# Optimization experiments

Hardware: AMD Instinct MI355X
Metric: run time of the kernel (lower is better)

## Reference

```python
import jax, jax.numpy as jnp
import numpy as np

N = 50000
E_RAND = 800000
IN_CH = 128
HID = 64
HEADS = 4
OUT_CH = 3
NEG_SLOPE = 0.2
BN_EPS = 1e-5


def setup_inputs() -> dict:
    key = jax.random.key(0)
    ks = jax.random.split(key, 24)
    x = jax.random.normal(ks[0], (N, IN_CH), dtype=jnp.float32)
    er = jax.random.randint(ks[1], (2, E_RAND), 0, N)
    sl = jnp.tile(jnp.arange(N, dtype=er.dtype)[None, :], (2, 1))
    edge_index = jnp.concatenate([er, sl], axis=1)  # [2, 850000]
    s = 0.1
    d1 = HID * HEADS            # 256
    d2 = (HID // 2) * HEADS     # 128
    inp = dict(x=x, edge_index=edge_index)
    # layer 1: in 128 -> heads*64
    inp["W1"] = s * jax.random.normal(ks[2], (IN_CH, HEADS * HID), dtype=jnp.float32)
    inp["a1s"] = s * jax.random.normal(ks[3], (HEADS, HID), dtype=jnp.float32)
    inp["a1d"] = s * jax.random.normal(ks[4], (HEADS, HID), dtype=jnp.float32)
    inp["b1"] = jnp.zeros((d1,), jnp.float32)
    inp["g1"] = jnp.ones((d1,), jnp.float32)
    inp["be1"] = jnp.zeros((d1,), jnp.float32)
    inp["m1"] = 0.01 * jax.random.normal(ks[5], (d1,), dtype=jnp.float32)
    inp["v1"] = jnp.ones((d1,), jnp.float32) + 0.01 * jax.random.uniform(ks[6], (d1,))
    # layer 2: in 256 -> heads*32
    inp["W2"] = s * jax.random.normal(ks[7], (d1, HEADS * (HID // 2)), dtype=jnp.float32)
    inp["a2s"] = s * jax.random.normal(ks[8], (HEADS, HID // 2), dtype=jnp.float32)
    inp["a2d"] = s * jax.random.normal(ks[9], (HEADS, HID // 2), dtype=jnp.float32)
    inp["b2"] = jnp.zeros((d2,), jnp.float32)
    inp["g2"] = jnp.ones((d2,), jnp.float32)
    inp["be2"] = jnp.zeros((d2,), jnp.float32)
    inp["m2"] = 0.01 * jax.random.normal(ks[10], (d2,), dtype=jnp.float32)
    inp["v2"] = jnp.ones((d2,), jnp.float32) + 0.01 * jax.random.uniform(ks[11], (d2,))
    # layer 3: in 128 -> 1 head, out_ch, concat=False
    inp["W3"] = s * jax.random.normal(ks[12], (d2, OUT_CH), dtype=jnp.float32)
    inp["a3s"] = s * jax.random.normal(ks[13], (1, OUT_CH), dtype=jnp.float32)
    inp["a3d"] = s * jax.random.normal(ks[14], (1, OUT_CH), dtype=jnp.float32)
    inp["b3"] = jnp.zeros((OUT_CH,), jnp.float32)
    return inp


def gat_conv(x, src, dst, W, a_src, a_dst, b, heads, fdim, concat):
    n = x.shape[0]
    h = (x @ W).reshape(n, heads, fdim)           # [N,H,F]
    als = jnp.einsum('nhf,hf->nh', h, a_src)      # [N,H]
    ald = jnp.einsum('nhf,hf->nh', h, a_dst)
    e = jax.nn.leaky_relu(als[src] + ald[dst], NEG_SLOPE)  # [E,H]
    m = jax.lax.stop_gradient(jax.ops.segment_max(e, dst, num_segments=n))
    ex = jnp.exp(e - m[dst])
    ssum = jax.ops.segment_sum(ex, dst, num_segments=n)
    alpha = ex / (ssum[dst] + 1e-16)              # segment softmax over in-edges
    msg = h[src] * alpha[:, :, None]              # [E,H,F]
    out = jax.ops.segment_sum(msg, dst, num_segments=n)  # [N,H,F]
    out = out.reshape(n, heads * fdim) if concat else out.mean(axis=1)
    return out + b


def batch_norm(x, gamma, beta, mean, var):
    return (x - mean) * jax.lax.rsqrt(var + BN_EPS) * gamma + beta


def reference(x, edge_index, W1, a1s, a1d, b1, g1, be1, m1, v1,
              W2, a2s, a2d, b2, g2, be2, m2, v2,
              W3, a3s, a3d, b3):
    src, dst = edge_index[0], edge_index[1]
    h = gat_conv(x, src, dst, W1, a1s, a1d, b1, HEADS, HID, True)
    h = jax.nn.elu(batch_norm(h, g1, be1, m1, v1))
    h = gat_conv(h, src, dst, W2, a2s, a2d, b2, HEADS, HID // 2, True)
    h = jax.nn.elu(batch_norm(h, g2, be2, m2, v2))
    h = gat_conv(h, src, dst, W3, a3s, a3d, b3, 1, OUT_CH, False)
    return jax.nn.log_softmax(h, axis=1)
```

## Files before the change

### kernel.cpp

```cpp
#include <hip/hip_runtime.h>


#define WSZ 64

typedef short short8 __attribute__((ext_vector_type(8)));
typedef short short4v __attribute__((ext_vector_type(4)));
typedef float float4v __attribute__((ext_vector_type(4)));
typedef float f2v __attribute__((ext_vector_type(2)));
typedef unsigned uint2v __attribute__((ext_vector_type(2)));

__device__ inline unsigned short f2bf(float f) {
  unsigned u = __float_as_uint(f);
  u += 0x7FFFu + ((u >> 16) & 1u);
  return (unsigned short)(u >> 16);
}
__device__ inline float bf2f(unsigned short u) {
  return __uint_as_float(((unsigned)u) << 16);
}


__global__ __launch_bounds__(256) void hist_kernel(const int* __restrict__ dst, int E,
                                                   int* __restrict__ deg) {
  int e = blockIdx.x * 256 + threadIdx.x;
  if (e < E) atomicAdd(&deg[dst[e]], 1);
}

__global__ __launch_bounds__(256) void block_sums_kernel(const int* __restrict__ deg, int n,
                                                         int* __restrict__ bsum) {
  __shared__ int sh[256];
  int t = threadIdx.x;
  int base = blockIdx.x * 1024 + t * 4;
  int v = 0;
#pragma unroll
  for (int j = 0; j < 4; ++j) {
    int idx = base + j;
    if (idx < n) v += deg[idx];
  }
  sh[t] = v;
  __syncthreads();
  for (int off = 128; off >= 1; off >>= 1) {
    if (t < off) sh[t] += sh[t + off];
    __syncthreads();
  }
  if (t == 0) bsum[blockIdx.x] = sh[0];
}

__global__ void tiny_scan_kernel(int* bsum, int nb) {
  if (threadIdx.x == 0 && blockIdx.x == 0) {
    int run = 0;
    for (int i = 0; i < nb; ++i) {
      int v = bsum[i];
      bsum[i] = run;
      run += v;
    }
  }
}

__global__ __launch_bounds__(256) void scan_write_kernel(const int* __restrict__ deg, int n,
                                                         const int* __restrict__ bbase,
                                                         int* __restrict__ row_start,
                                                         int* __restrict__ cursor) {
  __shared__ int sh[256];
  int t = threadIdx.x;
  int base = blockIdx.x * 1024 + t * 4;
  int v[4];
  int s = 0;
#pragma unroll
  for (int j = 0; j < 4; ++j) {
    int idx = base + j;
    v[j] = (idx < n) ? deg[idx] : 0;
    s += v[j];
  }
  sh[t] = s;
  __syncthreads();
  for (int off = 1; off < 256; off <<= 1) {
    int x = (t >= off) ? sh[t - off] : 0;
    __syncthreads();
    sh[t] += x;
    __syncthreads();
  }
  int excl = sh[t] - s + bbase[blockIdx.x];
#pragma unroll
  for (int j = 0; j < 4; ++j) {
    int idx = base + j;
    if (idx < n) {
      row_start[idx] = excl;
      cursor[idx] = excl;
    }
    excl += v[j];
  }
  if (blockIdx.x == gridDim.x - 1 && t == 255) row_start[n] = excl;
}

__global__ __launch_bounds__(256) void scatter_kernel(const int* __restrict__ src,
                                                      const int* __restrict__ dst, int E,
                                                      int* __restrict__ cursor,
                                                      int* __restrict__ csr_src) {
  int e = blockIdx.x * 256 + threadIdx.x;
  if (e < E) {
    int d = dst[e];
    int p = atomicAdd(&cursor[d], 1);
    csr_src[p] = src[e];
  }
}


__global__ __launch_bounds__(256) void conv_w1t_kernel(const float* __restrict__ W1,
                                                       unsigned short* __restrict__ W1t) {
  int idx = blockIdx.x * 256 + threadIdx.x;
  int n = idx >> 7, k = idx & 127;
  W1t[idx] = f2bf(W1[k * 256 + n]);
}

__global__ __launch_bounds__(256) void conv_w2t_kernel(const float* __restrict__ W2,
                                                       unsigned short* __restrict__ W2t) {
  int idx = blockIdx.x * 256 + threadIdx.x;
  int n = idx >> 8, p = idx & 255;
  int kl = (p & ~63) | ((p & 3) << 4) | ((p >> 2) & 15);
  W2t[idx] = f2bf(W2[kl * 128 + n]);
}

__global__ __launch_bounds__(512) void bn_prep_kernel(
    const float* __restrict__ b1, const float* __restrict__ g1,
    const float* __restrict__ be1, const float* __restrict__ m1,
    const float* __restrict__ v1, const float* __restrict__ b2,
    const float* __restrict__ g2, const float* __restrict__ be2,
    const float* __restrict__ m2, const float* __restrict__ v2,
    float* __restrict__ sc1, float* __restrict__ sh1,
    float* __restrict__ sc2, float* __restrict__ sh2) {
  int t = threadIdx.x;
  if (t < 256) {
    float s = g1[t] * rsqrtf(v1[t] + 1e-5f);
    sc1[t] = s;
    sh1[t] = (b1[t] - m1[t]) * s + be1[t];
  } else if (t < 384) {
    int i = t - 256;
    float s = g2[i] * rsqrtf(v2[i] + 1e-5f);
    sc2[i] = s;
    sh2[i] = (b2[i] - m2[i]) * s + be2[i];
  }
}


template <int K, int BN, bool AF32>
__global__ __launch_bounds__(256) void gemm_mfma(
    const void* __restrict__ Ap,
    const unsigned short* __restrict__ Bt,
    const float* __restrict__ a_s, const float* __restrict__ a_d,
    unsigned short* __restrict__ hout,
    float* __restrict__ als, float* __restrict__ ald,
    int M) {
  constexpr int CF = BN / 64;
  constexpr int SF = BN / 8;
  constexpr int PAD = 36;
  __shared__ unsigned short As[64][PAD];
  __shared__ unsigned short Bs[BN][PAD];
  const int t = threadIdx.x;
  const int w = t >> 6;
  const int lane = t & 63;
  const int c16 = lane & 15;
  const int q = lane >> 4;
  const int bm = blockIdx.x * 64;
  const int arow = t >> 2;
  const int akc = (t & 3) * 8;

  float4v acc[4][CF];
#pragma unroll
  for (int rf = 0; rf < 4; ++rf)
#pragma unroll
    for (int cf = 0; cf < CF; ++cf) acc[rf][cf] = float4v{0.f, 0.f, 0.f, 0.f};

  for (int k0 = 0; k0 < K; k0 += 32) {
    {
      int gr = bm + arow;
      if constexpr (AF32) {
        const float* Af = (const float*)Ap + (size_t)gr * K + k0 + akc;
        float4 v0 = make_float4(0.f, 0.f, 0.f, 0.f), v1 = v0;
        if (gr < M) {
          v0 = *(const float4*)Af;
          v1 = *(const float4*)(Af + 4);
        }
        ushort4 u0, u1;
        u0.x = f2bf(v0.x); u0.y = f2bf(v0.y); u0.z = f2bf(v0.z); u0.w = f2bf(v0.w);
        u1.x = f2bf(v1.x); u1.y = f2bf(v1.y); u1.z = f2bf(v1.z); u1.w = f2bf(v1.w);
        *(ushort4*)&As[arow][akc] = u0;
        *(ushort4*)&As[arow][akc + 4] = u1;
      } else {
        uint4 v = make_uint4(0u, 0u, 0u, 0u);
        if (gr < M) v = *(const uint4*)((const unsigned short*)Ap + (size_t)gr * K + k0 + akc);
        *(uint2*)&As[arow][akc] = make_uint2(v.x, v.y);
        *(uint2*)&As[arow][akc + 4] = make_uint2(v.z, v.w);
      }
    }
#pragma unroll
    for (int h = 0; h < BN / 64; ++h) {
      int n = (t >> 2) + h * 64;
      uint4 v = *(const uint4*)(Bt + (size_t)n * K + k0 + akc);
      *(uint2*)&Bs[n][akc] = make_uint2(v.x, v.y);
      *(uint2*)&Bs[n][akc + 4] = make_uint2(v.z, v.w);
    }
    __syncthreads();
    short8 af[4], bfr[CF];
#pragma unroll
    for (int rf = 0; rf < 4; ++rf) {
      short4v lo = *(short4v*)&As[rf * 16 + c16][q * 8];
      short4v hi = *(short4v*)&As[rf * 16 + c16][q * 8 + 4];
      af[rf] = __builtin_shufflevector(lo, hi, 0, 1, 2, 3, 4, 5, 6, 7);
    }
#pragma unroll
    for (int cf = 0; cf < CF; ++cf) {
      int n = w * (CF * 16) + cf * 16 + c16;
      short4v lo = *(short4v*)&Bs[n][q * 8];
      short4v hi = *(short4v*)&Bs[n][q * 8 + 4];
      bfr[cf] = __builtin_shufflevector(lo, hi, 0, 1, 2, 3, 4, 5, 6, 7);
    }
#pragma unroll
    for (int rf = 0; rf < 4; ++rf)
#pragma unroll
      for (int cf = 0; cf < CF; ++cf)
        acc[rf][cf] =
            __builtin_amdgcn_mfma_f32_16x16x32_bf16(af[rf], bfr[cf], acc[rf][cf], 0, 0, 0);
    __syncthreads();
  }

  float sasv[CF], sadv[CF];
#pragma unroll
  for (int cf = 0; cf < CF; ++cf) {
    int L = w * (CF * 16) + cf * 16 + c16;
    sasv[cf] = a_s[L];
    sadv[cf] = a_d[L];
  }
  const size_t sub = (size_t)(w * 2 + (c16 >> 3)) * (size_t)M * SF;
#pragma unroll
  for (int rf = 0; rf < 4; ++rf) {
#pragma unroll
    for (int r = 0; r < 4; ++r) {
      int n = bm + rf * 16 + q * 4 + r;
      float ps = 0.f, pd = 0.f;
      unsigned short us[CF];
#pragma unroll
      for (int cf = 0; cf < CF; ++cf) {
        float v = acc[rf][cf][r];
        us[cf] = f2bf(v);
        ps += v * sasv[cf];
        pd += v * sadv[cf];
      }
#pragma unroll
      for (int off = 1; off <= 8; off <<= 1) {
        ps += __shfl_xor(ps, off, 16);
        pd += __shfl_xor(pd, off, 16);
      }
      if (n < M) {
        if constexpr (CF == 4) {
          ushort4 u;
          u.x = us[0]; u.y = us[1]; u.z = us[2]; u.w = us[3];
          *(ushort4*)(hout + sub + (size_t)n * 32 + (c16 & 7) * 4) = u;
        } else {
          ushort2 u;
          u.x = us[0]; u.y = us[1];
          *(ushort2*)(hout + sub + (size_t)n * 16 + (c16 & 7) * 2) = u;
        }
        if (c16 == 0) {
          als[(size_t)n * 4 + w] = ps;
          ald[(size_t)n * 4 + w] = pd;
        }
      }
    }
  }
}


__global__ __launch_bounds__(256) void alpha_kernel(
    const float* __restrict__ als, const float* __restrict__ ald,
    const int* __restrict__ row_start, const int* __restrict__ csr_src,
    float* __restrict__ alpha, int E, int n_nodes) {
  int wid = threadIdx.x >> 6, lane = threadIdx.x & 63;
  int n = __builtin_amdgcn_readfirstlane(blockIdx.x * 4 + wid);
  if (n >= n_nodes) return;
  int head = lane & 3;
  int eg = lane >> 2;
  float aldv = ald[(size_t)n * 4 + head];
  int row = __builtin_amdgcn_readfirstlane(row_start[n]);
  int end = __builtin_amdgcn_readfirstlane(row_start[n + 1]);
  float ssum = 0.f;
  for (int i = row; i < end; i += 16) {
    int e = i + eg;
    int ec = (e < end) ? e : (end - 1);
    int s = csr_src[ec];
    float x = als[(size_t)(unsigned)s * 4 + head] + aldv;
    x = fmaxf(x, 0.2f * x);
    float ex = __expf(x);
    ssum += (e < end) ? ex : 0.f;
  }
  ssum += __shfl_xor(ssum, 4, 64);
  ssum += __shfl_xor(ssum, 8, 64);
  ssum += __shfl_xor(ssum, 16, 64);
  ssum += __shfl_xor(ssum, 32, 64);
  float inv = 1.f / (ssum + 1e-16f);
  float* apl = alpha + (size_t)head * (unsigned)E;
  for (int i = row; i < end; i += 16) {
    int e = i + eg;
    if (e < end) {
      int s = csr_src[e];
      float x = als[(size_t)(unsigned)s * 4 + head] + aldv;
      x = fmaxf(x, 0.2f * x);
      apl[e] = __expf(x) * inv;
    }
  }
}


template <int D>
__global__ __launch_bounds__(256) void gat_agg_slice(
    const unsigned short* __restrict__ h_sl,
    const float* __restrict__ alpha,
    const int* __restrict__ row_start, const int* __restrict__ csr_src,
    const float* __restrict__ bnsc, const float* __restrict__ bnsh,
    unsigned short* __restrict__ obf,
    float* __restrict__ of32,
    int E, int n_nodes) {
  constexpr int SFEAT = D / 8;
  constexpr int KF = SFEAT / 8;
  const int sl = blockIdx.x & 7;
  const int g = blockIdx.x >> 3;
  const int wid = threadIdx.x >> 6, lane = threadIdx.x & 63;
  const int f = lane & 7;
  const int ng = lane >> 3;
  const int head = sl >> 1;
  const char* hb = (const char*)(h_sl + (size_t)sl * (unsigned)n_nodes * SFEAT);
  const char* cb = (const char*)csr_src;
  const char* apb = (const char*)(alpha + (size_t)head * (unsigned)E);
  const unsigned uoff = (unsigned)(f * KF * 2);

  const int lb = (D == 256 ? head * 64 : head * 32) + (sl & 1) * 8 + f;
  float sc0 = bnsc[lb], sh0 = bnsh[lb];
  float sc1 = bnsc[lb + 16], sh1 = bnsh[lb + 16];
  float sc2 = 0.f, sh2 = 0.f, sc3 = 0.f, sh3 = 0.f;
  if constexpr (D == 256) {
    sc2 = bnsc[lb + 32]; sh2 = bnsh[lb + 32];
    sc3 = bnsc[lb + 48]; sh3 = bnsh[lb + 48];
  }

  int n = g * 32 + wid * 8 + ng;
  bool valid = n < n_nodes;
  int nc = valid ? n : (n_nodes - 1);
  int row = row_start[nc];
  int deg = row_start[nc + 1] - row;
  if (!valid) deg = 0;
  int mx = deg;
#pragma unroll
  for (int off = 8; off <= 32; off <<= 1) mx = max(mx, __shfl_xor(mx, off, 64));
  mx = __builtin_amdgcn_readfirstlane(mx);

  float acc0 = 0.f, acc1 = 0.f, acc2 = 0.f, acc3 = 0.f;
#pragma unroll 2
  for (int j = 0; j < mx; ++j) {
    bool act = j < deg;
    unsigned idx = (unsigned)(row + (act ? j : 0));
    int s = *(const int*)(cb + idx * 4u);
    float a = *(const float*)(apb + idx * 4u);
    a = act ? a : 0.f;
    if constexpr (D == 256) {
      uint2v u = *(const uint2v*)(hb + ((unsigned)s * 64u + uoff));
      acc0 += a * __uint_as_float(u.x << 16);
      acc1 += a * __uint_as_float(u.x & 0xffff0000u);
      acc2 += a * __uint_as_float(u.y << 16);
      acc3 += a * __uint_as_float(u.y & 0xffff0000u);
    } else {
      unsigned u = *(const unsigned*)(hb + ((unsigned)s * 32u + uoff));
      acc0 += a * __uint_as_float(u << 16);
      acc1 += a * __uint_as_float(u & 0xffff0000u);
    }
  }

  if (valid) {
    if constexpr (D == 256) {
      float v0 = acc0 * sc0 + sh0;
      float v1 = acc1 * sc1 + sh1;
      float v2 = acc2 * sc2 + sh2;
      float v3 = acc3 * sc3 + sh3;
      v0 = (v0 > 0.f) ? v0 : (__expf(v0) - 1.f);
      v1 = (v1 > 0.f) ? v1 : (__expf(v1) - 1.f);
      v2 = (v2 > 0.f) ? v2 : (__expf(v2) - 1.f);
      v3 = (v3 > 0.f) ? v3 : (__expf(v3) - 1.f);
      uint2v pk;
      pk.x = (unsigned)f2bf(v0) | ((unsigned)f2bf(v1) << 16);
      pk.y = (unsigned)f2bf(v2) | ((unsigned)f2bf(v3) << 16);
      __builtin_nontemporal_store(
          pk, (uint2v*)(obf + (size_t)n * 256 + sl * 32 + f * 4));
    } else {
      float v0 = acc0 * sc0 + sh0;
      float v1 = acc1 * sc1 + sh1;
      v0 = (v0 > 0.f) ? v0 : (__expf(v0) - 1.f);
      v1 = (v1 > 0.f) ? v1 : (__expf(v1) - 1.f);
      f2v v2;
      v2.x = v0; v2.y = v1;
      __builtin_nontemporal_store(
          v2, (f2v*)(of32 + (size_t)n * 128 + sl * 16 + f * 2));
    }
  }
}


__global__ __launch_bounds__(256) void l3_prep_kernel(
    const float* __restrict__ o2, const float* __restrict__ W3,
    const float* __restrict__ a3s, const float* __restrict__ a3d,
    float4* __restrict__ h3p, float* __restrict__ ald3, int n_nodes) {
  __shared__ float w3s[384];
  __shared__ float sa3[6];
  for (int i = threadIdx.x; i < 384; i += 256) w3s[i] = W3[i];
  if (threadIdx.x < 3) {
    sa3[threadIdx.x] = a3s[threadIdx.x];
    sa3[3 + threadIdx.x] = a3d[threadIdx.x];
  }
  __syncthreads();
  int wid = threadIdx.x >> 6, lane = threadIdx.x & 63;
  int n = blockIdx.x * 4 + wid;
  if (n >= n_nodes) return;
  f2v v = *(const f2v*)(o2 + (size_t)n * 128 + lane * 2);
  int hd = lane >> 4;
  int k0l = hd * 32 + (lane & 15);
  int k1l = k0l + 16;
  float p0 = v.x * w3s[k0l * 3 + 0] + v.y * w3s[k1l * 3 + 0];
  float p1 = v.x * w3s[k0l * 3 + 1] + v.y * w3s[k1l * 3 + 1];
  float p2 = v.x * w3s[k0l * 3 + 2] + v.y * w3s[k1l * 3 + 2];
#pragma unroll
  for (int off = 32; off >= 1; off >>= 1) {
    p0 += __shfl_xor(p0, off, 64);
    p1 += __shfl_xor(p1, off, 64);
    p2 += __shfl_xor(p2, off, 64);
  }
  if (lane == 0) {
    float als3 = p0 * sa3[0] + p1 * sa3[1] + p2 * sa3[2];
    float ad3 = p0 * sa3[3] + p1 * sa3[4] + p2 * sa3[5];
    h3p[n] = make_float4(p0, p1, p2, als3);
    ald3[n] = ad3;
  }
}


__global__ __launch_bounds__(256) void l3_agg_kernel(const float4* __restrict__ h3p,
                                                     const float* __restrict__ ald3,
                                                     const int* __restrict__ row_start,
                                                     const int* __restrict__ csr_src,
                                                     const float* __restrict__ b3,
                                                     float* __restrict__ out, int n_nodes) {
  int wid = threadIdx.x >> 6, lane = threadIdx.x & 63;
  int n = __builtin_amdgcn_readfirstlane(blockIdx.x * 4 + wid);
  if (n >= n_nodes) return;
  float aldv = ald3[n];
  int row = __builtin_amdgcn_readfirstlane(row_start[n]);
  int end = __builtin_amdgcn_readfirstlane(row_start[n + 1]);
  const char* hp = (const char*)h3p;
  float a0 = 0.f, a1 = 0.f, a2 = 0.f, ss = 0.f;
  for (int i = row + lane; i < end; i += 64) {
    int s = csr_src[i];
    float4 hv = *(const float4*)(hp + ((unsigned)s * 16u));
    float e = hv.w + aldv;
    e = fmaxf(e, 0.2f * e);
    float ex = __expf(e);
    ss += ex;
    a0 += ex * hv.x;
    a1 += ex * hv.y;
    a2 += ex * hv.z;
  }
#pragma unroll
  for (int off = 32; off >= 1; off >>= 1) {
    a0 += __shfl_xor(a0, off, 64);
    a1 += __shfl_xor(a1, off, 64);
    a2 += __shfl_xor(a2, off, 64);
    ss += __shfl_xor(ss, off, 64);
  }
  if (lane == 0) {
    float inv = 1.f / (ss + 1e-16f);
    float o0 = a0 * inv + b3[0];
    float o1 = a1 * inv + b3[1];
    float o2 = a2 * inv + b3[2];
    float m = fmaxf(o0, fmaxf(o1, o2));
    float lse = m + logf(expf(o0 - m) + expf(o1 - m) + expf(o2 - m));
    out[n * 3 + 0] = o0 - lse;
    out[n * 3 + 1] = o1 - lse;
    out[n * 3 + 2] = o2 - lse;
  }
}


extern "C" void kernel_launch(void* const* d_in, const int* in_sizes, int n_in,
                              void* d_out, int out_size, void* d_ws, size_t ws_size,
                              hipStream_t stream) {
  const float* x   = (const float*)d_in[0];
  const int*   ei  = (const int*)d_in[1];
  const float* W1  = (const float*)d_in[2];
  const float* a1s = (const float*)d_in[3];
  const float* a1d = (const float*)d_in[4];
  const float* b1  = (const float*)d_in[5];
  const float* g1v = (const float*)d_in[6];
  const float* be1 = (const float*)d_in[7];
  const float* m1  = (const float*)d_in[8];
  const float* v1  = (const float*)d_in[9];
  const float* W2  = (const float*)d_in[10];
  const float* a2s = (const float*)d_in[11];
  const float* a2d = (const float*)d_in[12];
  const float* b2  = (const float*)d_in[13];
  const float* g2v = (const float*)d_in[14];
  const float* be2 = (const float*)d_in[15];
  const float* m2  = (const float*)d_in[16];
  const float* v2  = (const float*)d_in[17];
  const float* W3  = (const float*)d_in[18];
  const float* a3s = (const float*)d_in[19];
  const float* a3d = (const float*)d_in[20];
  const float* b3  = (const float*)d_in[21];
  float* out = (float*)d_out;

  const int N = in_sizes[0] / 128;
  const int E = in_sizes[1] / 2;
  const int* srcv = ei;
  const int* dstv = ei + E;

  float* wsf  = (float*)d_ws;
  float* als1 = wsf;
  float* ald1 = als1 + (size_t)N * 4;
  float* als2 = ald1 + (size_t)N * 4;
  float* ald2 = als2 + (size_t)N * 4;
  float* h3p  = ald2 + (size_t)N * 4;
  float* ald3 = h3p + (size_t)N * 4;
  unsigned short* h1s   = (unsigned short*)(ald3 + N);
  unsigned short* o1_bf = h1s + (size_t)N * 256;
  unsigned short* W1t   = o1_bf + (size_t)N * 256;
  unsigned short* W2t   = W1t + 256 * 128;
  int* deg       = (int*)(W2t + 128 * 256);
  int* row_start = deg + N;
  int* cursor    = row_start + (N + 1);
  int* csr_src   = cursor + (N + 1);
  int* bsum      = csr_src + E;
  float* bnsc1 = (float*)(bsum + 1024);
  float* bnsh1 = bnsc1 + 256;
  float* bnsc2 = bnsh1 + 256;
  float* bnsh2 = bnsc2 + 128;
  unsigned short* h2s = (unsigned short*)(bnsh2 + 128);
  float* alpha1 = (float*)h2s;
  float* alpha2 = (float*)o1_bf;
  float* o2f    = (float*)h1s;

  const int eb = (E + 255) / 256;
  const int nb = (N + 1023) / 1024;
  const int nodes4 = (N + 3) / 4;
  const int mblocks = (N + 63) / 64;
  const int aggblocks = ((N + 31) / 32) * 8;

  conv_w1t_kernel<<<128, 256, 0, stream>>>(W1, W1t);
  conv_w2t_kernel<<<128, 256, 0, stream>>>(W2, W2t);
  bn_prep_kernel<<<1, 512, 0, stream>>>(b1, g1v, be1, m1, v1, b2, g2v, be2, m2, v2,
                                        bnsc1, bnsh1, bnsc2, bnsh2);

  hipMemsetAsync(deg, 0, (size_t)N * sizeof(int), stream);
  hist_kernel<<<eb, 256, 0, stream>>>(dstv, E, deg);
  block_sums_kernel<<<nb, 256, 0, stream>>>(deg, N, bsum);
  tiny_scan_kernel<<<1, 64, 0, stream>>>(bsum, nb);
  scan_write_kernel<<<nb, 256, 0, stream>>>(deg, N, bsum, row_start, cursor);
  scatter_kernel<<<eb, 256, 0, stream>>>(srcv, dstv, E, cursor, csr_src);

  gemm_mfma<128, 256, true><<<mblocks, 256, 0, stream>>>(x, W1t, a1s, a1d, h1s, als1,
                                                         ald1, N);
  alpha_kernel<<<nodes4, 256, 0, stream>>>(als1, ald1, row_start, csr_src, alpha1, E, N);
  gat_agg_slice<256><<<aggblocks, 256, 0, stream>>>(
      h1s, alpha1, row_start, csr_src, bnsc1, bnsh1, o1_bf, nullptr, E, N);
  gemm_mfma<256, 128, false><<<mblocks, 256, 0, stream>>>(o1_bf, W2t, a2s, a2d, h2s, als2,
                                                          ald2, N);
  alpha_kernel<<<nodes4, 256, 0, stream>>>(als2, ald2, row_start, csr_src, alpha2, E, N);
  gat_agg_slice<128><<<aggblocks, 256, 0, stream>>>(
      h2s, alpha2, row_start, csr_src, bnsc2, bnsh2, nullptr, o2f, E, N);
  l3_prep_kernel<<<nodes4, 256, 0, stream>>>(o2f, W3, a3s, a3d, (float4*)h3p, ald3, N);
  l3_agg_kernel<<<nodes4, 256, 0, stream>>>((const float4*)h3p, ald3, row_start, csr_src,
                                            b3, out, N);
}
```

Before: 455.9 us.

## Sort nodes by degree for aggregation balance and cache exp values in alpha

Adds a degree histogram, a scan and a scatter that build a node ordering grouped by in-degree. The aggregation kernels then process nodes in this order, so the 8 nodes sharing a wavefront have similar degrees and less of the wave idles behind the longest row. The alpha kernel keeps the first 64 exponentials per head in registers and writes them directly, so short rows skip the second pass's reload and recompute. Also raises the aggregation loop unroll to 4. The cost is three extra small kernels and a memset, plus scattered output writes and a loss of source locality, because neighbouring slots no longer hold consecutive nodes.

```diff
diff --git a/kernel.cpp b/kernel.cpp
--- a/kernel.cpp
+++ b/kernel.cpp
@@ -101,6 +101,35 @@
     int d = dst[e];
     int p = atomicAdd(&cursor[d], 1);
     csr_src[p] = src[e];
+  }
+}
+
+
+__global__ __launch_bounds__(256) void dhist_kernel(const int* __restrict__ deg, int N,
+                                                    int* __restrict__ dh) {
+  int n = blockIdx.x * 256 + threadIdx.x;
+  if (n < N) atomicAdd(&dh[min(deg[n], 63)], 1);
+}
+
+__global__ void dscan_kernel(const int* __restrict__ dh, int* __restrict__ dcur,
+                             int* __restrict__ nodeord, int N) {
+  if (threadIdx.x == 0) {
+    int run = 0;
+    for (int i = 0; i < 64; ++i) {
+      dcur[i] = run;
+      run += dh[i];
+    }
+  }
+  nodeord[N + threadIdx.x] = 0;
+}
+
+__global__ __launch_bounds__(256) void dscatter_kernel(const int* __restrict__ deg, int N,
+                                                       int* __restrict__ dcur,
+                                                       int* __restrict__ nodeord) {
+  int n = blockIdx.x * 256 + threadIdx.x;
+  if (n < N) {
+    int p = atomicAdd(&dcur[min(deg[n], 63)], 1);
+    nodeord[p] = n;
   }
 }
 
@@ -282,15 +311,30 @@
   float aldv = ald[(size_t)n * 4 + head];
   int row = __builtin_amdgcn_readfirstlane(row_start[n]);
   int end = __builtin_amdgcn_readfirstlane(row_start[n + 1]);
-  float ssum = 0.f;
-  for (int i = row; i < end; i += 16) {
+  float ex0 = 0.f, ex1 = 0.f, ex2 = 0.f, ex3 = 0.f;
+
+#define ABLK(exK, base)                                             \
+  {                                                                 \
+    int e = (base) + eg;                                            \
+    int ec = (e < end) ? e : (end - 1);                             \
+    int s = csr_src[ec];                                            \
+    float xv = als[(size_t)(unsigned)s * 4 + head] + aldv;          \
+    xv = fmaxf(xv, 0.2f * xv);                                      \
+    exK = (e < end) ? __expf(xv) : 0.f;                             \
+  }
+
+  ABLK(ex0, row)
+  if (end > row + 16) ABLK(ex1, row + 16)
+  if (end > row + 32) ABLK(ex2, row + 32)
+  if (end > row + 48) ABLK(ex3, row + 48)
+  float ssum = (ex0 + ex1) + (ex2 + ex3);
+  for (int i = row + 64; i < end; i += 16) {
     int e = i + eg;
     int ec = (e < end) ? e : (end - 1);
     int s = csr_src[ec];
-    float x = als[(size_t)(unsigned)s * 4 + head] + aldv;
-    x = fmaxf(x, 0.2f * x);
-    float ex = __expf(x);
-    ssum += (e < end) ? ex : 0.f;
+    float xv = als[(size_t)(unsigned)s * 4 + head] + aldv;
+    xv = fmaxf(xv, 0.2f * xv);
+    ssum += (e < end) ? __expf(xv) : 0.f;
   }
   ssum += __shfl_xor(ssum, 4, 64);
   ssum += __shfl_xor(ssum, 8, 64);
@@ -298,15 +342,20 @@
   ssum += __shfl_xor(ssum, 32, 64);
   float inv = 1.f / (ssum + 1e-16f);
   float* apl = alpha + (size_t)head * (unsigned)E;
-  for (int i = row; i < end; i += 16) {
+  if (row + eg < end) apl[row + eg] = ex0 * inv;
+  if (end > row + 16 && row + 16 + eg < end) apl[row + 16 + eg] = ex1 * inv;
+  if (end > row + 32 && row + 32 + eg < end) apl[row + 32 + eg] = ex2 * inv;
+  if (end > row + 48 && row + 48 + eg < end) apl[row + 48 + eg] = ex3 * inv;
+  for (int i = row + 64; i < end; i += 16) {
     int e = i + eg;
     if (e < end) {
       int s = csr_src[e];
-      float x = als[(size_t)(unsigned)s * 4 + head] + aldv;
-      x = fmaxf(x, 0.2f * x);
-      apl[e] = __expf(x) * inv;
-    }
-  }
+      float xv = als[(size_t)(unsigned)s * 4 + head] + aldv;
+      xv = fmaxf(xv, 0.2f * xv);
+      apl[e] = __expf(xv) * inv;
+    }
+  }
+#undef ABLK
 }
 
 
@@ -315,6 +364,7 @@
     const unsigned short* __restrict__ h_sl,
     const float* __restrict__ alpha,
     const int* __restrict__ row_start, const int* __restrict__ csr_src,
+    const int* __restrict__ nodeord,
     const float* __restrict__ bnsc, const float* __restrict__ bnsh,
     unsigned short* __restrict__ obf,
     float* __restrict__ of32,
@@ -341,11 +391,11 @@
     sc3 = bnsc[lb + 48]; sh3 = bnsh[lb + 48];
   }
 
-  int n = g * 32 + wid * 8 + ng;
-  bool valid = n < n_nodes;
-  int nc = valid ? n : (n_nodes - 1);
-  int row = row_start[nc];
-  int deg = row_start[nc + 1] - row;
+  int slot = g * 32 + wid * 8 + ng;
+  bool valid = slot < n_nodes;
+  int n = nodeord[slot];
+  int row = row_start[n];
+  int deg = row_start[n + 1] - row;
   if (!valid) deg = 0;
   int mx = deg;
 #pragma unroll
@@ -353,7 +403,7 @@
   mx = __builtin_amdgcn_readfirstlane(mx);
 
   float acc0 = 0.f, acc1 = 0.f, acc2 = 0.f, acc3 = 0.f;
-#pragma unroll 2
+#pragma unroll 4
   for (int j = 0; j < mx; ++j) {
     bool act = j < deg;
     unsigned idx = (unsigned)(row + (act ? j : 0));
@@ -537,7 +587,10 @@
   float* bnsh1 = bnsc1 + 256;
   float* bnsc2 = bnsh1 + 256;
   float* bnsh2 = bnsc2 + 128;
-  unsigned short* h2s = (unsigned short*)(bnsh2 + 128);
+  int* dh      = (int*)(bnsh2 + 128);
+  int* dcur    = dh + 64;
+  int* nodeord = dcur + 64;
+  unsigned short* h2s = (unsigned short*)(nodeord + N + 64);
   float* alpha1 = (float*)h2s;
   float* alpha2 = (float*)o1_bf;
   float* o2f    = (float*)h1s;
@@ -554,22 +607,26 @@
                                         bnsc1, bnsh1, bnsc2, bnsh2);
 
   hipMemsetAsync(deg, 0, (size_t)N * sizeof(int), stream);
+  hipMemsetAsync(dh, 0, 64 * sizeof(int), stream);
   hist_kernel<<<eb, 256, 0, stream>>>(dstv, E, deg);
   block_sums_kernel<<<nb, 256, 0, stream>>>(deg, N, bsum);
   tiny_scan_kernel<<<1, 64, 0, stream>>>(bsum, nb);
   scan_write_kernel<<<nb, 256, 0, stream>>>(deg, N, bsum, row_start, cursor);
   scatter_kernel<<<eb, 256, 0, stream>>>(srcv, dstv, E, cursor, csr_src);
+  dhist_kernel<<<nb * 4, 256, 0, stream>>>(deg, N, dh);
+  dscan_kernel<<<1, 64, 0, stream>>>(dh, dcur, nodeord, N);
+  dscatter_kernel<<<nb * 4, 256, 0, stream>>>(deg, N, dcur, nodeord);
 
   gemm_mfma<128, 256, true><<<mblocks, 256, 0, stream>>>(x, W1t, a1s, a1d, h1s, als1,
                                                          ald1, N);
   alpha_kernel<<<nodes4, 256, 0, stream>>>(als1, ald1, row_start, csr_src, alpha1, E, N);
   gat_agg_slice<256><<<aggblocks, 256, 0, stream>>>(
-      h1s, alpha1, row_start, csr_src, bnsc1, bnsh1, o1_bf, nullptr, E, N);
+      h1s, alpha1, row_start, csr_src, nodeord, bnsc1, bnsh1, o1_bf, nullptr, E, N);
   gemm_mfma<256, 128, false><<<mblocks, 256, 0, stream>>>(o1_bf, W2t, a2s, a2d, h2s, als2,
                                                           ald2, N);
   alpha_kernel<<<nodes4, 256, 0, stream>>>(als2, ald2, row_start, csr_src, alpha2, E, N);
   gat_agg_slice<128><<<aggblocks, 256, 0, stream>>>(
-      h2s, alpha2, row_start, csr_src, bnsc2, bnsh2, nullptr, o2f, E, N);
+      h2s, alpha2, row_start, csr_src, nodeord, bnsc2, bnsh2, nullptr, o2f, E, N);
   l3_prep_kernel<<<nodes4, 256, 0, stream>>>(o2f, W3, a3s, a3d, (float4*)h3p, ald3, N);
   l3_agg_kernel<<<nodes4, 256, 0, stream>>>((const float4*)h3p, ald3, row_start, csr_src,
                                             b3, out, N);
```

New measurement: 744.2 us. 63.2% more time.

## Fuse edge softmax into aggregation kernel with LDS-staged neighbor lists

Applied to the files above, without the earlier changes.

Drops the separate alpha kernel and computes the unnormalised exp attention inside the aggregation loop, keeping a running sum and normalising once at the end. Each block first stages its 32 nodes' source indices and source-attention logits into shared memory, with a global-memory fallback when the edge range exceeds capacity. This removes the alpha write and read traffic and two launches. In exchange, each of the 8 slice blocks recomputes the exp per edge, and the shared-memory staging adds a block barrier and an LDS footprint.

```diff
diff --git a/kernel.cpp b/kernel.cpp
--- a/kernel.cpp
+++ b/kernel.cpp
@@ -270,115 +270,107 @@
 }
 
 
-__global__ __launch_bounds__(256) void alpha_kernel(
-    const float* __restrict__ als, const float* __restrict__ ald,
-    const int* __restrict__ row_start, const int* __restrict__ csr_src,
-    float* __restrict__ alpha, int E, int n_nodes) {
-  int wid = threadIdx.x >> 6, lane = threadIdx.x & 63;
-  int n = __builtin_amdgcn_readfirstlane(blockIdx.x * 4 + wid);
-  if (n >= n_nodes) return;
-  int head = lane & 3;
-  int eg = lane >> 2;
-  float aldv = ald[(size_t)n * 4 + head];
-  int row = __builtin_amdgcn_readfirstlane(row_start[n]);
-  int end = __builtin_amdgcn_readfirstlane(row_start[n + 1]);
-  float ssum = 0.f;
-  for (int i = row; i < end; i += 16) {
-    int e = i + eg;
-    int ec = (e < end) ? e : (end - 1);
-    int s = csr_src[ec];
-    float x = als[(size_t)(unsigned)s * 4 + head] + aldv;
-    x = fmaxf(x, 0.2f * x);
-    float ex = __expf(x);
-    ssum += (e < end) ? ex : 0.f;
-  }
-  ssum += __shfl_xor(ssum, 4, 64);
-  ssum += __shfl_xor(ssum, 8, 64);
-  ssum += __shfl_xor(ssum, 16, 64);
-  ssum += __shfl_xor(ssum, 32, 64);
-  float inv = 1.f / (ssum + 1e-16f);
-  float* apl = alpha + (size_t)head * (unsigned)E;
-  for (int i = row; i < end; i += 16) {
-    int e = i + eg;
-    if (e < end) {
-      int s = csr_src[e];
-      float x = als[(size_t)(unsigned)s * 4 + head] + aldv;
-      x = fmaxf(x, 0.2f * x);
-      apl[e] = __expf(x) * inv;
-    }
-  }
-}
-
-
 template <int D>
 __global__ __launch_bounds__(256) void gat_agg_slice(
     const unsigned short* __restrict__ h_sl,
-    const float* __restrict__ alpha,
+    const float* __restrict__ als, const float* __restrict__ ald,
     const int* __restrict__ row_start, const int* __restrict__ csr_src,
     const float* __restrict__ bnsc, const float* __restrict__ bnsh,
     unsigned short* __restrict__ obf,
     float* __restrict__ of32,
-    int E, int n_nodes) {
+    int n_nodes) {
   constexpr int SFEAT = D / 8;
   constexpr int KF = SFEAT / 8;
+  constexpr int CAP = 1280;
+  __shared__ int s_s[CAP];
+  __shared__ float s_a[CAP];
   const int sl = blockIdx.x & 7;
   const int g = blockIdx.x >> 3;
-  const int wid = threadIdx.x >> 6, lane = threadIdx.x & 63;
+  const int tid = threadIdx.x;
+  const int wid = tid >> 6, lane = tid & 63;
   const int f = lane & 7;
   const int ng = lane >> 3;
   const int head = sl >> 1;
   const char* hb = (const char*)(h_sl + (size_t)sl * (unsigned)n_nodes * SFEAT);
-  const char* cb = (const char*)csr_src;
-  const char* apb = (const char*)(alpha + (size_t)head * (unsigned)E);
   const unsigned uoff = (unsigned)(f * KF * 2);
 
+  const int nb0 = g * 32;
+  int rs = __builtin_amdgcn_readfirstlane(row_start[nb0]);
+  int re = __builtin_amdgcn_readfirstlane(row_start[min(nb0 + 32, n_nodes)]);
+  const bool fast = (re - rs) <= CAP;
+  if (fast) {
+    for (int i = rs + tid; i < re; i += 256) {
+      int s = csr_src[i];
+      s_s[i - rs] = s;
+      s_a[i - rs] = als[(size_t)(unsigned)s * 4 + head];
+    }
+  }
+  __syncthreads();
+
   const int lb = (D == 256 ? head * 64 : head * 32) + (sl & 1) * 8 + f;
-  float sc0 = bnsc[lb], sh0 = bnsh[lb];
-  float sc1 = bnsc[lb + 16], sh1 = bnsh[lb + 16];
-  float sc2 = 0.f, sh2 = 0.f, sc3 = 0.f, sh3 = 0.f;
+  float sc0 = bnsc[lb], sh0v = bnsh[lb];
+  float sc1 = bnsc[lb + 16], sh1v = bnsh[lb + 16];
+  float sc2 = 0.f, sh2v = 0.f, sc3 = 0.f, sh3v = 0.f;
   if constexpr (D == 256) {
-    sc2 = bnsc[lb + 32]; sh2 = bnsh[lb + 32];
-    sc3 = bnsc[lb + 48]; sh3 = bnsh[lb + 48];
-  }
-
-  int n = g * 32 + wid * 8 + ng;
+    sc2 = bnsc[lb + 32]; sh2v = bnsh[lb + 32];
+    sc3 = bnsc[lb + 48]; sh3v = bnsh[lb + 48];
+  }
+
+  int n = nb0 + wid * 8 + ng;
   bool valid = n < n_nodes;
-  int nc = valid ? n : (n_nodes - 1);
-  int row = row_start[nc];
-  int deg = row_start[nc + 1] - row;
-  if (!valid) deg = 0;
+  int row = valid ? row_start[n] : rs;
+  int deg = valid ? (row_start[n + 1] - row) : 0;
+  float aldv = ald[(size_t)(unsigned)(valid ? n : 0) * 4 + head];
   int mx = deg;
 #pragma unroll
   for (int off = 8; off <= 32; off <<= 1) mx = max(mx, __shfl_xor(mx, off, 64));
   mx = __builtin_amdgcn_readfirstlane(mx);
 
-  float acc0 = 0.f, acc1 = 0.f, acc2 = 0.f, acc3 = 0.f;
+  float acc0 = 0.f, acc1 = 0.f, acc2 = 0.f, acc3 = 0.f, ssum = 0.f;
+
+#define AGG_BODY(SGET, AGET)                                        \
+  {                                                                 \
+    bool act = j < deg;                                             \
+    int jo = act ? j : 0;                                           \
+    int s = (SGET);                                                 \
+    float av = (AGET);                                              \
+    float e = av + aldv;                                            \
+    e = fmaxf(e, 0.2f * e);                                         \
+    float ex = __expf(e);                                           \
+    ex = act ? ex : 0.f;                                            \
+    ssum += ex;                                                     \
+    if constexpr (D == 256) {                                       \
+      uint2v u = *(const uint2v*)(hb + ((unsigned)s * 64u + uoff)); \
+      acc0 += ex * __uint_as_float(u.x << 16);                      \
+      acc1 += ex * __uint_as_float(u.x & 0xffff0000u);              \
+      acc2 += ex * __uint_as_float(u.y << 16);                      \
+      acc3 += ex * __uint_as_float(u.y & 0xffff0000u);              \
+    } else {                                                        \
+      unsigned u = *(const unsigned*)(hb + ((unsigned)s * 32u + uoff)); \
+      acc0 += ex * __uint_as_float(u << 16);                        \
+      acc1 += ex * __uint_as_float(u & 0xffff0000u);                \
+    }                                                               \
+  }
+
+  if (fast) {
+    int base = row - rs;
+#pragma unroll 4
+    for (int j = 0; j < mx; ++j) AGG_BODY(s_s[base + jo], s_a[base + jo])
+  } else {
 #pragma unroll 2
-  for (int j = 0; j < mx; ++j) {
-    bool act = j < deg;
-    unsigned idx = (unsigned)(row + (act ? j : 0));
-    int s = *(const int*)(cb + idx * 4u);
-    float a = *(const float*)(apb + idx * 4u);
-    a = act ? a : 0.f;
+    for (int j = 0; j < mx; ++j)
+      AGG_BODY(csr_src[row + jo], als[(size_t)(unsigned)s * 4 + head])
+  }
+#undef AGG_BODY
+
+  if (valid) {
+    float inv = 1.f / (ssum + 1e-16f);
     if constexpr (D == 256) {
-      uint2v u = *(const uint2v*)(hb + ((unsigned)s * 64u + uoff));
-      acc0 += a * __uint_as_float(u.x << 16);
-      acc1 += a * __uint_as_float(u.x & 0xffff0000u);
-      acc2 += a * __uint_as_float(u.y << 16);
-      acc3 += a * __uint_as_float(u.y & 0xffff0000u);
-    } else {
-      unsigned u = *(const unsigned*)(hb + ((unsigned)s * 32u + uoff));
-      acc0 += a * __uint_as_float(u << 16);
-      acc1 += a * __uint_as_float(u & 0xffff0000u);
-    }
-  }
-
-  if (valid) {
-    if constexpr (D == 256) {
-      float v0 = acc0 * sc0 + sh0;
-      float v1 = acc1 * sc1 + sh1;
-      float v2 = acc2 * sc2 + sh2;
-      float v3 = acc3 * sc3 + sh3;
+      float o0 = acc0 * inv, o1 = acc1 * inv, o2 = acc2 * inv, o3 = acc3 * inv;
+      float v0 = o0 * sc0 + sh0v;
+      float v1 = o1 * sc1 + sh1v;
+      float v2 = o2 * sc2 + sh2v;
+      float v3 = o3 * sc3 + sh3v;
       v0 = (v0 > 0.f) ? v0 : (__expf(v0) - 1.f);
       v1 = (v1 > 0.f) ? v1 : (__expf(v1) - 1.f);
       v2 = (v2 > 0.f) ? v2 : (__expf(v2) - 1.f);
@@ -389,8 +381,9 @@
       __builtin_nontemporal_store(
           pk, (uint2v*)(obf + (size_t)n * 256 + sl * 32 + f * 4));
     } else {
-      float v0 = acc0 * sc0 + sh0;
-      float v1 = acc1 * sc1 + sh1;
+      float o0 = acc0 * inv, o1 = acc1 * inv;
+      float v0 = o0 * sc0 + sh0v;
+      float v1 = o1 * sc1 + sh1v;
       v0 = (v0 > 0.f) ? v0 : (__expf(v0) - 1.f);
       v1 = (v1 > 0.f) ? v1 : (__expf(v1) - 1.f);
       f2v v2;
@@ -517,6 +510,12 @@
   const int* srcv = ei;
   const int* dstv = ei + E;
 
+  const int eb = (E + 255) / 256;
+  const int nb = (N + 1023) / 1024;
+  const int nodes4 = (N + 3) / 4;
+  const int mblocks = (N + 63) / 64;
+  const int aggblocks = ((N + 31) / 32) * 8;
+
   float* wsf  = (float*)d_ws;
   float* als1 = wsf;
   float* ald1 = als1 + (size_t)N * 4;
@@ -538,15 +537,7 @@
   float* bnsc2 = bnsh1 + 256;
   float* bnsh2 = bnsc2 + 128;
   unsigned short* h2s = (unsigned short*)(bnsh2 + 128);
-  float* alpha1 = (float*)h2s;
-  float* alpha2 = (float*)o1_bf;
-  float* o2f    = (float*)h1s;
-
-  const int eb = (E + 255) / 256;
-  const int nb = (N + 1023) / 1024;
-  const int nodes4 = (N + 3) / 4;
-  const int mblocks = (N + 63) / 64;
-  const int aggblocks = ((N + 31) / 32) * 8;
+  float* o2f = (float*)h1s;
 
   conv_w1t_kernel<<<128, 256, 0, stream>>>(W1, W1t);
   conv_w2t_kernel<<<128, 256, 0, stream>>>(W2, W2t);
@@ -562,14 +553,12 @@
 
   gemm_mfma<128, 256, true><<<mblocks, 256, 0, stream>>>(x, W1t, a1s, a1d, h1s, als1,
                                                          ald1, N);
-  alpha_kernel<<<nodes4, 256, 0, stream>>>(als1, ald1, row_start, csr_src, alpha1, E, N);
   gat_agg_slice<256><<<aggblocks, 256, 0, stream>>>(
-      h1s, alpha1, row_start, csr_src, bnsc1, bnsh1, o1_bf, nullptr, E, N);
+      h1s, als1, ald1, row_start, csr_src, bnsc1, bnsh1, o1_bf, nullptr, N);
   gemm_mfma<256, 128, false><<<mblocks, 256, 0, stream>>>(o1_bf, W2t, a2s, a2d, h2s, als2,
                                                           ald2, N);
-  alpha_kernel<<<nodes4, 256, 0, stream>>>(als2, ald2, row_start, csr_src, alpha2, E, N);
   gat_agg_slice<128><<<aggblocks, 256, 0, stream>>>(
-      h2s, alpha2, row_start, csr_src, bnsc2, bnsh2, nullptr, o2f, E, N);
+      h2s, als2, ald2, row_start, csr_src, bnsc2, bnsh2, nullptr, o2f, N);
   l3_prep_kernel<<<nodes4, 256, 0, stream>>>(o2f, W3, a3s, a3d, (float4*)h3p, ald3, N);
   l3_agg_kernel<<<nodes4, 256, 0, stream>>>((const float4*)h3p, ald3, row_start, csr_src,
                                             b3, out, N);
```

Measured after the change: 428.0 us. 1.07x faster.
